# Optimization experiments

Measured on AMD Instinct MI355X. Metric: run time of the kernel, lower is better.

## Reference

```python
import jax, jax.numpy as jnp
import numpy as np
from jax import lax

B, H, W, C = 4, 1024, 1024, 3
NF = 21                 # n_sampled_fields
GH, GW = 8, 8           # psf_grid_shape
PSF_H, PSF_W = 65, 65   # sampled psf shape
RPSF = 23               # resized psf (0.26mm extent / ~0.011mm pixel pitch)
HALF_DIAG = float(np.hypot(H - 1, W - 1) / 2.0)

# ---------- static field / coordinate maps ----------
def _maps():
    ys = (np.arange(H, dtype=np.float32) - (H - 1) / 2.0) / HALF_DIAG
    xs = (np.arange(W, dtype=np.float32) - (W - 1) / 2.0) / HALF_DIAG
    x = np.broadcast_to(xs[None, :], (H, W))
    y = np.broadcast_to(ys[:, None], (H, W))
    r = np.sqrt(x * x + y * y)
    field_map = np.clip(r, 0.0, 1.0)
    return (jnp.asarray(x), jnp.asarray(y), jnp.asarray(field_map), xs, ys)

X_MAP, Y_MAP, FIELD_MAP, XS, YS = _maps()

# ---------- helpers faithful to the TF source ----------
def _lin_interp(soft_idx, values):
    soft_idx = jnp.clip(soft_idx, 0, values.shape[0] - 1)
    lo = jnp.floor(soft_idx).astype(jnp.int32)
    hi = jnp.ceil(soft_idx).astype(jnp.int32)
    f = soft_idx % 1
    return values[lo] * (1 - f) + values[hi] * f

def _psf_weights():
    # get_psf_weights: mean one-hot of discretized field over linspace patches
    ph = int(round(H / GH)); pw = int(round(W / GW))
    rows0 = np.round(np.linspace(0, 1, GH) * (H - ph)).astype(int)
    cols0 = np.round(np.linspace(0, 1, GW) * (W - pw)).astype(int)
    rows = rows0[:, None] + np.arange(ph)[None, :]   # [GH, ph]
    cols = cols0[:, None] + np.arange(pw)[None, :]   # [GW, pw]
    dfm = jnp.round(FIELD_MAP * (NF - 1)).astype(jnp.int32)
    patches = dfm[rows[:, None, :, None], cols[None, :, None, :]]  # [GH,GW,ph,pw]
    onehot = (patches[..., None] == jnp.arange(NF)).astype(jnp.float32)
    return onehot.mean(axis=(2, 3)).reshape(GH * GW, NF)  # [G, NF]

PSF_WEIGHTS = _psf_weights()

def _cell_angles():
    x0, x1 = XS[0], XS[-1]; y0, y1 = YS[0], YS[-1]
    xc = (np.arange(GW) + 0.5) / GW * (x1 - x0) + x0
    yc = (np.arange(GH) + 0.5) / GH * (y1 - y0) + y0
    return jnp.asarray(np.arctan2(xc[None, :], yc[:, None]).reshape(-1), jnp.float32)

ANGLES = _cell_angles()

def _rotate_bilinear(psf, angle):
    # psf [ph, pw, C]; counterclockwise rotation, zero fill outside
    ph, pw = psf.shape[:2]
    cy, cx = (ph - 1) / 2.0, (pw - 1) / 2.0
    ys, xs = jnp.meshgrid(jnp.arange(ph, dtype=jnp.float32),
                          jnp.arange(pw, dtype=jnp.float32), indexing='ij')
    ca, sa = jnp.cos(angle), jnp.sin(angle)
    sx = ca * (xs - cx) + sa * (ys - cy) + cx
    sy = -sa * (xs - cx) + ca * (ys - cy) + cy
    x0 = jnp.floor(sx).astype(jnp.int32); y0 = jnp.floor(sy).astype(jnp.int32)
    fx, fy = sx - x0, sy - y0
    def g(yi, xi):
        valid = (yi >= 0) & (yi < ph) & (xi >= 0) & (xi < pw)
        v = psf[jnp.clip(yi, 0, ph - 1), jnp.clip(xi, 0, pw - 1)]
        return jnp.where(valid[..., None], v, 0.0)
    return (g(y0, x0) * ((1 - fy) * (1 - fx))[..., None]
            + g(y0, x0 + 1) * ((1 - fy) * fx)[..., None]
            + g(y0 + 1, x0) * (fy * (1 - fx))[..., None]
            + g(y0 + 1, x0 + 1) * (fy * fx)[..., None])

def _cubic_w(t):
    # Keys bicubic kernel, a = -0.5 (matches interpolate_bicubic)
    a = -0.5
    t2 = t * t; t3 = t2 * t
    return jnp.where(t <= 1, (a + 2) * t3 - (a + 3) * t2 + 1,
                     jnp.where(t < 2, a * t3 - 5 * a * t2 + 8 * a * t - 4 * a, 0.0))

def _bicubic_warp(img, qx, qy):
    # img [H, W, K] flattened-channel image; qx, qy [HW] query pixel coords
    K = img.shape[-1]
    imgf = img.reshape(H * W, K)
    x0 = jnp.floor(qx).astype(jnp.int32); y0 = jnp.floor(qy).astype(jnp.int32)
    fx, fy = qx - x0, qy - y0
    out = jnp.zeros((H * W, K), img.dtype)
    for j in range(-1, 3):
        yj = jnp.clip(y0 + j, 0, H - 1)
        wy = _cubic_w(jnp.abs(fy - j))
        for i in range(-1, 3):
            xi = jnp.clip(x0 + i, 0, W - 1)
            wx = _cubic_w(jnp.abs(fx - i))
            out = out + (wy * wx)[:, None] * imgf[yj * W + xi]
    return out

# ---------- inputs ----------
def setup_inputs() -> dict:
    key = jax.random.key(0)
    k1, k2, k3, k4 = jax.random.split(key, 4)
    img = jax.random.uniform(k1, (B, H, W, C), jnp.float32)
    sampled_psfs = jax.random.uniform(k2, (NF, PSF_H, PSF_W, C), jnp.float32)
    sampled_distortion_shifts = 0.02 * jax.random.normal(k3, (NF,), jnp.float32)
    sampled_relative_illumination = 0.5 + 0.5 * jax.random.uniform(k4, (NF,), jnp.float32)
    return {"img": img, "sampled_psfs": sampled_psfs,
            "sampled_distortion_shifts": sampled_distortion_shifts,
            "sampled_relative_illumination": sampled_relative_illumination}

# ---------- forward ----------
def reference(img, sampled_psfs, sampled_distortion_shifts, sampled_relative_illumination):
    # 1) relative illumination (interpolate_relative_illumination)
    ri_map = _lin_interp(FIELD_MAP * (NF - 1), sampled_relative_illumination)
    img = img * ri_map[None, :, :, None]

    # 2) field-dependent PSFs: interpolate -> rotate -> resize -> normalize
    interp = jnp.einsum('gf,fhwc->ghwc', PSF_WEIGHTS, sampled_psfs)  # [G,65,65,C]
    rotated = jax.vmap(_rotate_bilinear)(interp, -ANGLES)
    resized = jax.image.resize(rotated, (GH * GW, RPSF, RPSF, C), 'linear', antialias=True)
    psfs = resized / jnp.sum(resized, axis=(1, 2), keepdims=True)   # [G,k,k,C]

    # 3) patch-wise depthwise convolution with the per-cell PSFs
    ph, pw = H // GH, W // GW
    patches = img.reshape(B, GH, ph, GW, pw, C).transpose(1, 3, 0, 2, 4, 5)
    patches = patches.reshape(GH * GW, B, ph, pw, C)
    def cell_conv(p, k):  # p [B,ph,pw,C], k [kh,kw,1,C]
        return lax.conv_general_dilated(p, k, (1, 1), 'SAME',
                                        dimension_numbers=('NHWC', 'HWIO', 'NHWC'),
                                        feature_group_count=C)
    blurred = jax.vmap(cell_conv)(patches, psfs[:, :, :, None, :])
    img = blurred.reshape(GH, GW, B, ph, pw, C).transpose(2, 0, 3, 1, 4, 5).reshape(B, H, W, C)

    # 4) distortion by bicubic warping (interpolate_distortion_shifts + warp)
    r = jnp.sqrt(X_MAP ** 2 + Y_MAP ** 2)
    ang = jnp.arctan2(Y_MAP, X_MAP)
    shift = _lin_interp(r * (NF - 1), sampled_distortion_shifts)
    yy, xx = jnp.meshgrid(jnp.arange(H, dtype=jnp.float32),
                          jnp.arange(W, dtype=jnp.float32), indexing='ij')
    qx = (xx + shift * jnp.cos(ang) * HALF_DIAG).reshape(-1)
    qy = (yy + shift * jnp.sin(ang) * HALF_DIAG).reshape(-1)
    imgw = img.transpose(1, 2, 0, 3).reshape(H, W, B * C)
    warped = _bicubic_warp(imgw, qx, qy)               # [HW, B*C]
    out = warped.reshape(H, W, B, C).transpose(2, 0, 1, 3)
    return out

if __name__ == '__main__':
    o = reference(**setup_inputs())
    print(o.shape, float(o.mean()))
```

## Files before the change

### kernel.cpp

```cpp
#include <hip/hip_runtime.h>
#include <math.h>

#define HD 723.3702371153271f
#define HW2 1048576

typedef float float4u __attribute__((ext_vector_type(4), aligned(4)));

__device__ __forceinline__ float lin21(const float* __restrict__ t, float soft) {
    soft = fminf(fmaxf(soft, 0.f), 20.f);
    float fl = floorf(soft);
    int lo = (int)fl;
    int hi = (int)ceilf(soft);
    float f = soft - fl;
    return t[lo] * (1.f - f) + t[hi] * f;
}

__global__ __launch_bounds__(256) void k0_ri(const float* __restrict__ img,
                                             const float* __restrict__ ri_tab,
                                             float* __restrict__ img_ri) {
    int t = blockIdx.x * 256 + threadIdx.x;
    int p0 = t * 4;
    int b = p0 >> 20;
    int rem = p0 & (HW2 - 1);
    int y = rem >> 10, x = rem & 1023;
    const float4* src = (const float4*)(img + (size_t)p0 * 3);
    float4 A = src[0], Bv = src[1], Cv = src[2];
    float yn = ((float)y - 511.5f) / HD;
    float ri[4];
    #pragma unroll
    for (int k = 0; k < 4; ++k) {
        float xn = ((float)(x + k) - 511.5f) / HD;
        float r = sqrtf(xn * xn + yn * yn);
        ri[k] = lin21(ri_tab, fminf(r, 1.f) * 20.f);
    }
    size_t base = ((size_t)(b * 3) << 20) + (size_t)y * 1024 + x;
    float4 r0 = {A.x * ri[0], A.w * ri[1], Bv.z * ri[2], Cv.y * ri[3]};
    float4 r1 = {A.y * ri[0], Bv.x * ri[1], Bv.w * ri[2], Cv.z * ri[3]};
    float4 r2 = {A.z * ri[0], Bv.y * ri[1], Cv.x * ri[2], Cv.w * ri[3]};
    *(float4*)(img_ri + base) = r0;
    *(float4*)(img_ri + base + HW2) = r1;
    *(float4*)(img_ri + base + 2 * (size_t)HW2) = r2;
}

__global__ __launch_bounds__(256) void k1a_rot(const float* __restrict__ spsfs,
                                               float* __restrict__ rot) {
    __shared__ __align__(16) float bufA[65 * 65 * 3];
    __shared__ int ihist[21];
    __shared__ float wts[21];
    int g = blockIdx.x;
    int gy = g >> 3, gx = g & 7;
    int tid = threadIdx.x;
    if (tid < 21) ihist[tid] = 0;
    __syncthreads();
    int cnt[21];
    #pragma unroll
    for (int f = 0; f < 21; ++f) cnt[f] = 0;
    for (int i = tid; i < 128 * 128; i += 256) {
        int py = i >> 7, px = i & 127;
        int yg = gy * 128 + py, xg = gx * 128 + px;
        float xn = ((float)xg - 511.5f) / HD;
        float yn = ((float)yg - 511.5f) / HD;
        float r = sqrtf(xn * xn + yn * yn);
        int fbin = (int)rintf(fminf(r, 1.f) * 20.f);
        #pragma unroll
        for (int f = 0; f < 21; ++f)
            cnt[f] += __popcll(__ballot(fbin == f));
    }
    if ((tid & 63) == 0) {
        #pragma unroll
        for (int f = 0; f < 21; ++f)
            if (cnt[f] > 0) atomicAdd(&ihist[f], cnt[f]);
    }
    __syncthreads();
    if (tid < 21) wts[tid] = (float)ihist[tid] * (1.f / 16384.f);
    __syncthreads();
    for (int i = tid; i < 65 * 65 * 3; i += 256) {
        float acc = 0.f;
        #pragma unroll
        for (int f = 0; f < 21; ++f) acc = fmaf(wts[f], spsfs[f * (65 * 65 * 3) + i], acc);
        bufA[i] = acc;
    }
    __syncthreads();
    float x0c = -511.5f / HD, span = 1023.0f / HD;
    float xc = ((float)gx + 0.5f) * 0.125f * span + x0c;
    float yc = ((float)gy + 0.5f) * 0.125f * span + x0c;
    float a = -atan2f(xc, yc);
    float ca = cosf(a), sa = sinf(a);
    float* rg = rot + (size_t)g * (65 * 65 * 3);
    for (int i = tid; i < 65 * 65; i += 256) {
        int y = i / 65;
        int x = i - y * 65;
        float dx = (float)x - 32.f, dy = (float)y - 32.f;
        float sx = ca * dx + sa * dy + 32.f;
        float sy = -sa * dx + ca * dy + 32.f;
        float fxf = floorf(sx), fyf = floorf(sy);
        int ix0 = (int)fxf, iy0 = (int)fyf;
        float fx = sx - fxf, fy = sy - fyf;
        float w00 = (1.f - fy) * (1.f - fx);
        float w01 = (1.f - fy) * fx;
        float w10 = fy * (1.f - fx);
        float w11 = fy * fx;
        bool vx0 = (ix0 >= 0) && (ix0 < 65);
        bool vx1 = (ix0 + 1 >= 0) && (ix0 + 1 < 65);
        bool vy0 = (iy0 >= 0) && (iy0 < 65);
        bool vy1 = (iy0 + 1 >= 0) && (iy0 + 1 < 65);
        int cx0 = min(max(ix0, 0), 64), cx1 = min(max(ix0 + 1, 0), 64);
        int cy0 = min(max(iy0, 0), 64), cy1 = min(max(iy0 + 1, 0), 64);
        #pragma unroll
        for (int c = 0; c < 3; ++c) {
            float v00 = (vy0 && vx0) ? bufA[(cy0 * 65 + cx0) * 3 + c] : 0.f;
            float v01 = (vy0 && vx1) ? bufA[(cy0 * 65 + cx1) * 3 + c] : 0.f;
            float v10 = (vy1 && vx0) ? bufA[(cy1 * 65 + cx0) * 3 + c] : 0.f;
            float v11 = (vy1 && vx1) ? bufA[(cy1 * 65 + cx1) * 3 + c] : 0.f;
            rg[i * 3 + c] = w00 * v00 + w01 * v01 + w10 * v10 + w11 * v11;
        }
    }
}

__global__ __launch_bounds__(256) void k1b_resize(const float* __restrict__ rot,
                                                  float* __restrict__ psfs_out) {
    __shared__ float tmp[65 * 23 * 3];
    __shared__ float out23[23 * 23 * 3];
    __shared__ float csum[3];
    const float INV = 65.f / 23.f;
    int g = blockIdx.x;
    int tid = threadIdx.x;
    const float* rg = rot + (size_t)g * (65 * 65 * 3);
    for (int i = tid; i < 65 * 23 * 3; i += 256) {
        int y = i / 69;
        int rem = i - y * 69;
        int ox = rem / 3;
        int c = rem - ox * 3;
        float center = ((float)ox + 0.5f) * INV - 0.5f;
        int ilo = max(0, (int)ceilf(center - INV));
        int ihi = min(64, (int)floorf(center + INV));
        float acc = 0.f, wsum = 0.f;
        for (int ix = ilo; ix <= ihi; ++ix) {
            float w = fmaxf(1.f - fabsf(center - (float)ix) / INV, 0.f);
            acc += w * rg[(y * 65 + ix) * 3 + c];
            wsum += w;
        }
        tmp[i] = acc / wsum;
    }
    __syncthreads();
    for (int i = tid; i < 23 * 23 * 3; i += 256) {
        int oy = i / 69;
        int rem = i - oy * 69;
        int ox = rem / 3;
        int c = rem - ox * 3;
        float center = ((float)oy + 0.5f) * INV - 0.5f;
        int ilo = max(0, (int)ceilf(center - INV));
        int ihi = min(64, (int)floorf(center + INV));
        float acc = 0.f, wsum = 0.f;
        for (int iy = ilo; iy <= ihi; ++iy) {
            float w = fmaxf(1.f - fabsf(center - (float)iy) / INV, 0.f);
            acc += w * tmp[iy * 69 + ox * 3 + c];
            wsum += w;
        }
        out23[i] = acc / wsum;
    }
    __syncthreads();
    if (tid < 192) {
        int c = tid >> 6;
        int l = tid & 63;
        float s = 0.f;
        for (int j = l; j < 529; j += 64) s += out23[j * 3 + c];
        #pragma unroll
        for (int off = 32; off > 0; off >>= 1) s += __shfl_down(s, off);
        if (l == 0) csum[c] = s;
    }
    __syncthreads();
    for (int i = tid; i < 23 * 23 * 3; i += 256) {
        int pix = i / 3;
        int c = i - pix * 3;
        psfs_out[((size_t)g * 3 + c) * 529 + pix] = out23[i] / csum[c];
    }
}

#define LSTRIDE 156
__global__ __launch_bounds__(256, 2) void k2_conv(const float* __restrict__ img_ri,
                                                  const float* __restrict__ psfs,
                                                  float* __restrict__ blurred) {
    __shared__ __align__(16) float s_img[54 * LSTRIDE];
    __shared__ __align__(16) float s_psf[23 * 24];
    int ytile = blockIdx.x;
    int g = blockIdx.y;
    int bc = blockIdx.z;
    int gy = g >> 3, gx = g & 7;
    int c = bc - (bc / 3) * 3;
    int tid = threadIdx.x;
    for (int i = tid; i < 23 * 24; i += 256) {
        int ky = i / 24, kx = i - ky * 24;
        s_psf[i] = (kx < 23) ? psfs[((size_t)g * 3 + c) * 529 + ky * 23 + kx] : 0.f;
    }
    const float* plane = img_ri + (size_t)bc * HW2;
    int py0 = ytile * 32 - 11;
    for (int i = tid; i < 54 * LSTRIDE; i += 256) {
        int r = i / LSTRIDE;
        int col = i - r * LSTRIDE;
        int py = py0 + r;
        int px = col - 11;
        float v = 0.f;
        if (py >= 0 && py < 128 && px >= 0 && px < 128)
            v = plane[(size_t)(gy * 128 + py) * 1024 + (gx * 128 + px)];
        s_img[i] = v;
    }
    __syncthreads();
    int tx = tid & 7, ty = tid >> 3;
    float acc[16] __attribute__((aligned(16)));
    #pragma unroll
    for (int i = 0; i < 16; ++i) acc[i] = 0.f;
    #pragma unroll 1
    for (int ky = 0; ky < 23; ++ky) {
        float wrow[24] __attribute__((aligned(16)));
        const float4* wr4 = (const float4*)&s_psf[ky * 24];
        #pragma unroll
        for (int j = 0; j < 6; ++j) ((float4*)wrow)[j] = wr4[j];
        float line[40] __attribute__((aligned(16)));
        const float* lrow = &s_img[(ty + ky) * LSTRIDE + tx * 16];
        #pragma unroll
        for (int j = 0; j < 10; ++j) ((float4*)line)[j] = *(const float4*)&lrow[j * 4];
        #pragma unroll
        for (int kx = 0; kx < 23; ++kx) {
            float w = wrow[kx];
            #pragma unroll
            for (int i = 0; i < 16; ++i) acc[i] = fmaf(line[kx + i], w, acc[i]);
        }
    }
    int Y = gy * 128 + ytile * 32 + ty;
    int Xb = gx * 128 + tx * 16;
    float* dst = blurred + (size_t)bc * HW2 + (size_t)Y * 1024 + Xb;
    #pragma unroll
    for (int j = 0; j < 4; ++j) *(float4*)&dst[j * 4] = ((float4*)acc)[j];
}

__device__ __forceinline__ float cub1(float t) { return (1.5f * t - 2.5f) * t * t + 1.f; }
__device__ __forceinline__ float cub2(float t) { return ((-0.5f * t + 2.5f) * t - 4.f) * t + 2.f; }

__global__ __launch_bounds__(256) void k3_warp(const float* __restrict__ blurred,
                                               const float* __restrict__ shifts,
                                               float* __restrict__ out) {
    int p = blockIdx.x * 256 + threadIdx.x;
    int y = p >> 10, x = p & 1023;
    float xn = ((float)x - 511.5f) / HD;
    float yn = ((float)y - 511.5f) / HD;
    float r = sqrtf(xn * xn + yn * yn);
    float shift = lin21(shifts, r * 20.f);
    float s = shift * HD / r;
    float qx = (float)x + s * xn;
    float qy = (float)y + s * yn;
    float fxf = floorf(qx), fyf = floorf(qy);
    int x0 = (int)fxf, y0 = (int)fyf;
    float fx = qx - fxf, fy = qy - fyf;
    float wxx[4] = {cub2(fx + 1.f), cub1(fx), cub1(1.f - fx), cub2(2.f - fx)};
    float wyy[4] = {cub2(fy + 1.f), cub1(fy), cub1(1.f - fy), cub2(2.f - fy)};
    float acc[12];
    #pragma unroll
    for (int q = 0; q < 12; ++q) acc[q] = 0.f;
    bool safe = (x0 >= 1) && (x0 <= 1020);
    if (safe) {
        #pragma unroll
        for (int j = 0; j < 4; ++j) {
            int yj = min(max(y0 - 1 + j, 0), 1023);
            const float* rowp = blurred + (size_t)yj * 1024 + (x0 - 1);
            float wj = wyy[j];
            #pragma unroll
            for (int q = 0; q < 12; ++q) {
                float4u v = *(const float4u*)(rowp + (size_t)q * HW2);
                float dot = fmaf(v.x, wxx[0], fmaf(v.y, wxx[1], fmaf(v.z, wxx[2], v.w * wxx[3])));
                acc[q] = fmaf(wj, dot, acc[q]);
            }
        }
    } else {
        #pragma unroll
        for (int j = 0; j < 4; ++j) {
            int yj = min(max(y0 - 1 + j, 0), 1023);
            const float* rowp = blurred + (size_t)yj * 1024;
            #pragma unroll
            for (int i2 = 0; i2 < 4; ++i2) {
                int xi = min(max(x0 - 1 + i2, 0), 1023);
                float w = wyy[j] * wxx[i2];
                #pragma unroll
                for (int q = 0; q < 12; ++q)
                    acc[q] = fmaf(w, rowp[(size_t)q * HW2 + xi], acc[q]);
            }
        }
    }
    #pragma unroll
    for (int b = 0; b < 4; ++b) {
        size_t base = ((size_t)b * HW2 + (size_t)p) * 3;
        out[base] = acc[b * 3];
        out[base + 1] = acc[b * 3 + 1];
        out[base + 2] = acc[b * 3 + 2];
    }
}

extern "C" void kernel_launch(void* const* d_in, const int* in_sizes, int n_in,
                              void* d_out, int out_size, void* d_ws, size_t ws_size,
                              hipStream_t stream) {
    const float* img = (const float*)d_in[0];
    const float* spsfs = (const float*)d_in[1];
    const float* shifts = (const float*)d_in[2];
    const float* ritab = (const float*)d_in[3];
    float* out = (float*)d_out;

    char* ws = (char*)d_ws;
    float* psfs = (float*)(ws);
    float* rot = (float*)(ws + (size_t)524288);
    float* img_ri = (float*)(ws + (size_t)4194304);
    float* blurred = (float*)(ws + (size_t)4194304 + 50331648);

    k0_ri<<<4096, 256, 0, stream>>>(img, ritab, img_ri);
    k1a_rot<<<64, 256, 0, stream>>>(spsfs, rot);
    k1b_resize<<<64, 256, 0, stream>>>(rot, psfs);
    k2_conv<<<dim3(4, 64, 12), 256, 0, stream>>>(img_ri, psfs, blurred);
    k3_warp<<<4096, 256, 0, stream>>>(blurred, shifts, out);
}
```

Measured before the change: 483.3 us.

## Fuse relative-illumination scaling into conv tile load and drop separate pass

The standalone kernel that multiplied the image by the relative-illumination falloff and wrote a channel-planar copy is removed. The conv kernel now reads the interleaved NHWC input directly, computes the radial falloff per pixel while filling its shared-memory tile, and applies it on load. This removes a full-image write and read of the intermediate buffer. The cost is strided 3-channel gathers and recomputed sqrt/interp in the halo load. The thread-to-output mapping also swaps so ty varies fastest within a wavefront.

```diff
diff --git a/kernel.cpp b/kernel.cpp
--- a/kernel.cpp
+++ b/kernel.cpp
@@ -13,33 +13,6 @@
     int hi = (int)ceilf(soft);
     float f = soft - fl;
     return t[lo] * (1.f - f) + t[hi] * f;
-}
-
-__global__ __launch_bounds__(256) void k0_ri(const float* __restrict__ img,
-                                             const float* __restrict__ ri_tab,
-                                             float* __restrict__ img_ri) {
-    int t = blockIdx.x * 256 + threadIdx.x;
-    int p0 = t * 4;
-    int b = p0 >> 20;
-    int rem = p0 & (HW2 - 1);
-    int y = rem >> 10, x = rem & 1023;
-    const float4* src = (const float4*)(img + (size_t)p0 * 3);
-    float4 A = src[0], Bv = src[1], Cv = src[2];
-    float yn = ((float)y - 511.5f) / HD;
-    float ri[4];
-    #pragma unroll
-    for (int k = 0; k < 4; ++k) {
-        float xn = ((float)(x + k) - 511.5f) / HD;
-        float r = sqrtf(xn * xn + yn * yn);
-        ri[k] = lin21(ri_tab, fminf(r, 1.f) * 20.f);
-    }
-    size_t base = ((size_t)(b * 3) << 20) + (size_t)y * 1024 + x;
-    float4 r0 = {A.x * ri[0], A.w * ri[1], Bv.z * ri[2], Cv.y * ri[3]};
-    float4 r1 = {A.y * ri[0], Bv.x * ri[1], Bv.w * ri[2], Cv.z * ri[3]};
-    float4 r2 = {A.z * ri[0], Bv.y * ri[1], Cv.x * ri[2], Cv.w * ri[3]};
-    *(float4*)(img_ri + base) = r0;
-    *(float4*)(img_ri + base + HW2) = r1;
-    *(float4*)(img_ri + base + 2 * (size_t)HW2) = r2;
 }
 
 __global__ __launch_bounds__(256) void k1a_rot(const float* __restrict__ spsfs,
@@ -178,7 +151,8 @@
 }
 
 #define LSTRIDE 156
-__global__ __launch_bounds__(256, 2) void k2_conv(const float* __restrict__ img_ri,
+__global__ __launch_bounds__(256, 2) void k2_conv(const float* __restrict__ img,
+                                                  const float* __restrict__ ri_tab,
                                                   const float* __restrict__ psfs,
                                                   float* __restrict__ blurred) {
     __shared__ __align__(16) float s_img[54 * LSTRIDE];
@@ -187,13 +161,14 @@
     int g = blockIdx.y;
     int bc = blockIdx.z;
     int gy = g >> 3, gx = g & 7;
-    int c = bc - (bc / 3) * 3;
+    int b = bc / 3;
+    int c = bc - b * 3;
     int tid = threadIdx.x;
     for (int i = tid; i < 23 * 24; i += 256) {
         int ky = i / 24, kx = i - ky * 24;
         s_psf[i] = (kx < 23) ? psfs[((size_t)g * 3 + c) * 529 + ky * 23 + kx] : 0.f;
     }
-    const float* plane = img_ri + (size_t)bc * HW2;
+    const float* bimg = img + (size_t)b * (3 * (size_t)HW2);
     int py0 = ytile * 32 - 11;
     for (int i = tid; i < 54 * LSTRIDE; i += 256) {
         int r = i / LSTRIDE;
@@ -201,12 +176,18 @@
         int py = py0 + r;
         int px = col - 11;
         float v = 0.f;
-        if (py >= 0 && py < 128 && px >= 0 && px < 128)
-            v = plane[(size_t)(gy * 128 + py) * 1024 + (gx * 128 + px)];
+        if (py >= 0 && py < 128 && px >= 0 && px < 128) {
+            int yg = gy * 128 + py, xg = gx * 128 + px;
+            float xn = ((float)xg - 511.5f) / HD;
+            float yn = ((float)yg - 511.5f) / HD;
+            float rr = sqrtf(xn * xn + yn * yn);
+            float ri = lin21(ri_tab, fminf(rr, 1.f) * 20.f);
+            v = bimg[((size_t)yg * 1024 + xg) * 3 + c] * ri;
+        }
         s_img[i] = v;
     }
     __syncthreads();
-    int tx = tid & 7, ty = tid >> 3;
+    int ty = tid & 31, tx = tid >> 5;
     float acc[16] __attribute__((aligned(16)));
     #pragma unroll
     for (int i = 0; i < 16; ++i) acc[i] = 0.f;
@@ -307,12 +288,10 @@
     char* ws = (char*)d_ws;
     float* psfs = (float*)(ws);
     float* rot = (float*)(ws + (size_t)524288);
-    float* img_ri = (float*)(ws + (size_t)4194304);
-    float* blurred = (float*)(ws + (size_t)4194304 + 50331648);
-
-    k0_ri<<<4096, 256, 0, stream>>>(img, ritab, img_ri);
+    float* blurred = (float*)(ws + (size_t)4194304);
+
     k1a_rot<<<64, 256, 0, stream>>>(spsfs, rot);
     k1b_resize<<<64, 256, 0, stream>>>(rot, psfs);
-    k2_conv<<<dim3(4, 64, 12), 256, 0, stream>>>(img_ri, psfs, blurred);
+    k2_conv<<<dim3(4, 64, 12), 256, 0, stream>>>(img, ritab, psfs, blurred);
     k3_warp<<<4096, 256, 0, stream>>>(blurred, shifts, out);
 }
```

New measurement: 432.8 us. -10.4%, faster.
